# Kernel tuning notes

Measured on AMD Instinct MI355X. Metric: run time of the kernel, lower is better.

The kernel has to match this reference:

```python
import jax, jax.numpy as jnp
import numpy as np

N_NODES = 100000
N_EDGES = 600000
DIM_IN = 128
DIM_OUT = 40
N_LAYERS = 3


def setup_inputs() -> dict:
    key = jax.random.key(0)
    ks = jax.random.split(key, 6)
    x = jax.random.normal(ks[0], (N_NODES, DIM_IN), dtype=jnp.float32)
    edge_index = jax.random.randint(ks[1], (2, N_EDGES), 0, N_NODES, dtype=jnp.int64)
    eps = jnp.zeros((N_LAYERS,), dtype=jnp.float32)
    Ws = jax.random.normal(ks[2], (N_LAYERS, DIM_IN, DIM_IN), dtype=jnp.float32) * 0.08
    bs = jnp.zeros((N_LAYERS, DIM_IN), dtype=jnp.float32)
    W_head = jax.random.normal(ks[3], (DIM_IN, DIM_OUT), dtype=jnp.float32) * 0.08
    b_head = jnp.zeros((DIM_OUT,), dtype=jnp.float32)
    return {"x": x, "edge_index": edge_index, "eps": eps, "Ws": Ws,
            "bs": bs, "W_head": W_head, "b_head": b_head}


def reference(x, edge_index, eps, Ws, bs, W_head, b_head):
    # GINConv (train_eps): x' = Linear((1+eps)*x + sum_{j->i} x_j)
    src, dst = edge_index[0], edge_index[1]
    n = x.shape[0]
    for l in range(N_LAYERS):
        agg = jax.ops.segment_sum(x[src], dst, num_segments=n)  # scatter-add over edges
        x = ((1.0 + eps[l]) * x + agg) @ Ws[l] + bs[l]
        # dropout is identity in eval mode
    return x @ W_head + b_head  # node-level head Linear(dim_in, dim_out)
```

## Files before the change

kernel.cpp:

```cpp
#include <hip/hip_runtime.h>

#define DIM 128
#define NOUT 40

typedef __attribute__((ext_vector_type(8))) short bf16x8_t;
typedef __attribute__((ext_vector_type(4))) float f32x4_t;
typedef __attribute__((ext_vector_type(4))) unsigned u32x4_t;

__device__ __forceinline__ ushort f2bf(float f) {
    unsigned u = __float_as_uint(f);
    u += 0x7fffu + ((u >> 16) & 1u);
    return (ushort)(u >> 16);
}


__global__ __launch_bounds__(256) void hist_kernel(
    const int* __restrict__ dst, int* __restrict__ deg, int n_edges)
{
    int e = blockIdx.x * 256 + threadIdx.x;
    if (e < n_edges) atomicAdd(&deg[dst[e]], 1);
}

__global__ __launch_bounds__(256) void reduce_kernel(
    const int* __restrict__ deg, int* __restrict__ bsum, int n)
{
    int t = threadIdx.x;
    int base = blockIdx.x * 1024 + t;
    int s = 0;
    #pragma unroll
    for (int i = 0; i < 4; ++i) { int idx = base + i * 256; s += (idx < n) ? deg[idx] : 0; }
    for (int o = 32; o; o >>= 1) s += __shfl_down(s, o, 64);
    __shared__ int l[4];
    if ((t & 63) == 0) l[t >> 6] = s;
    __syncthreads();
    if (t == 0) bsum[blockIdx.x] = l[0] + l[1] + l[2] + l[3];
}

__global__ __launch_bounds__(128) void scan_sums_kernel(
    int* __restrict__ bsum, int nb, int* __restrict__ off_n)
{
    __shared__ int l[128];
    int t = threadIdx.x;
    int c = (nb + 127) >> 7;
    int b = t * c, e = min(b + c, nb);
    int s = 0;
    for (int i = b; i < e; ++i) s += bsum[i];
    l[t] = s;
    __syncthreads();
    for (int d = 1; d < 128; d <<= 1) {
        int u = (t >= d) ? l[t - d] : 0;
        __syncthreads();
        l[t] += u;
        __syncthreads();
    }
    int pre = l[t] - s;
    for (int i = b; i < e; ++i) { int v = bsum[i]; bsum[i] = pre; pre += v; }
    if (t == 127) *off_n = l[127];
}

__global__ __launch_bounds__(256) void apply_kernel(
    const int* __restrict__ deg, const int* __restrict__ bsum,
    int* __restrict__ off, int n)
{
    int t = threadIdx.x;
    int i0 = blockIdx.x * 1024 + t * 4;
    int d0 = (i0     < n) ? deg[i0]     : 0;
    int d1 = (i0 + 1 < n) ? deg[i0 + 1] : 0;
    int d2 = (i0 + 2 < n) ? deg[i0 + 2] : 0;
    int d3 = (i0 + 3 < n) ? deg[i0 + 3] : 0;
    int s = d0 + d1 + d2 + d3;
    int inc = s;
    for (int o = 1; o < 64; o <<= 1) {
        int u = __shfl_up(inc, o, 64);
        if ((t & 63) >= o) inc += u;
    }
    __shared__ int wt[4];
    if ((t & 63) == 63) wt[t >> 6] = inc;
    __syncthreads();
    int wpre = 0;
    #pragma unroll
    for (int i = 0; i < 4; ++i) wpre += (i < (t >> 6)) ? wt[i] : 0;
    int excl = bsum[blockIdx.x] + wpre + inc - s;
    if (i0     < n) off[i0]     = excl;
    if (i0 + 1 < n) off[i0 + 1] = excl + d0;
    if (i0 + 2 < n) off[i0 + 2] = excl + d0 + d1;
    if (i0 + 3 < n) off[i0 + 3] = excl + d0 + d1 + d2;
}

__global__ __launch_bounds__(256) void fill_kernel(
    const int* __restrict__ src, const int* __restrict__ dst,
    const int* __restrict__ off, int* __restrict__ cursor,
    int* __restrict__ csr_src, int n_edges)
{
    int e = blockIdx.x * 256 + threadIdx.x;
    if (e >= n_edges) return;
    int d = dst[e];
    int pos = off[d] + atomicAdd(&cursor[d], 1);
    csr_src[pos] = src[e];
}


__global__ __launch_bounds__(256) void cast_x_kernel(
    const float* __restrict__ x, ushort* __restrict__ xb, int n4)
{
    int i = blockIdx.x * 256 + threadIdx.x;
    if (i >= n4) return;
    float4 v = reinterpret_cast<const float4*>(x)[i];
    reinterpret_cast<ushort4*>(xb)[i] =
        make_ushort4(f2bf(v.x), f2bf(v.y), f2bf(v.z), f2bf(v.w));
}

__global__ __launch_bounds__(256) void pack_w_kernel(
    const float* __restrict__ Ws, const float* __restrict__ Wh,
    ushort* __restrict__ pW, ushort* __restrict__ pWh)
{
    int tid = blockIdx.x * 256 + threadIdx.x;
    if (tid < 3 * 16384) {
        int l = tid / 16384, r = tid % 16384;
        int j = r & 7, lane = (r >> 3) & 63, cb = (r >> 9) & 7, ks = r >> 12;
        int k  = ks * 32 + (lane >> 4) * 8 + j;
        int nn = cb * 16 + (lane & 15);
        pW[tid] = f2bf(Ws[(size_t)l * DIM * DIM + (size_t)k * DIM + nn]);
    } else {
        int r = tid - 3 * 16384;
        if (r < 4 * 3 * 64 * 8) {
            int j = r & 7, lane = (r >> 3) & 63;
            int rem = r >> 9;
            int cb = rem % 3, ks = rem / 3;
            int k  = ks * 32 + (lane >> 4) * 8 + j;
            int nn = cb * 16 + (lane & 15);
            pWh[r] = (nn < NOUT) ? f2bf(Wh[(size_t)k * NOUT + nn]) : (ushort)0;
        }
    }
}

template<bool HEAD>
__global__ __launch_bounds__(256) void gin_fused_mfma(
    const ushort* __restrict__ xb,
    const int* __restrict__ csr, const int* __restrict__ off,
    const ushort* __restrict__ pW, const float* __restrict__ bias,
    const ushort* __restrict__ pWh, const float* __restrict__ bh,
    const float* __restrict__ eps, int layer,
    ushort* __restrict__ Y, float* __restrict__ out, int n_nodes)
{
    __shared__ ushort lds[4][16][136];

    const int t = threadIdx.x, wave = t >> 6, lane = t & 63;
    const int rloc = lane & 15;
    const int kseg = lane >> 4;
    const int row16 = blockIdx.x * 64 + wave * 16;
    const int node  = row16 + rloc;
    const int nclamp = min(node, n_nodes - 1);
    const float e1 = 1.0f + eps[layer];

    float a[4][8];
    {
        const ushort* xr = xb + (size_t)nclamp * DIM + kseg * 8;
        #pragma unroll
        for (int s = 0; s < 4; ++s) {
            u32x4_t v = *reinterpret_cast<const u32x4_t*>(xr + s * 32);
            #pragma unroll
            for (int q = 0; q < 4; ++q) {
                a[s][2*q]   = e1 * __uint_as_float(v[q] << 16);
                a[s][2*q+1] = e1 * __uint_as_float(v[q] & 0xffff0000u);
            }
        }
    }
    int k = off[nclamp], ke = off[nclamp + 1];
    for (; k + 1 < ke; k += 2) {
        const ushort* r0 = xb + (size_t)csr[k]     * DIM + kseg * 8;
        const ushort* r1 = xb + (size_t)csr[k + 1] * DIM + kseg * 8;
        u32x4_t u0[4], u1[4];
        #pragma unroll
        for (int s = 0; s < 4; ++s) u0[s] = *reinterpret_cast<const u32x4_t*>(r0 + s * 32);
        #pragma unroll
        for (int s = 0; s < 4; ++s) u1[s] = *reinterpret_cast<const u32x4_t*>(r1 + s * 32);
        #pragma unroll
        for (int s = 0; s < 4; ++s)
            #pragma unroll
            for (int q = 0; q < 4; ++q) {
                a[s][2*q]   += __uint_as_float(u0[s][q] << 16)
                             + __uint_as_float(u1[s][q] << 16);
                a[s][2*q+1] += __uint_as_float(u0[s][q] & 0xffff0000u)
                             + __uint_as_float(u1[s][q] & 0xffff0000u);
            }
    }
    if (k < ke) {
        const ushort* r0 = xb + (size_t)csr[k] * DIM + kseg * 8;
        #pragma unroll
        for (int s = 0; s < 4; ++s) {
            u32x4_t v = *reinterpret_cast<const u32x4_t*>(r0 + s * 32);
            #pragma unroll
            for (int q = 0; q < 4; ++q) {
                a[s][2*q]   += __uint_as_float(v[q] << 16);
                a[s][2*q+1] += __uint_as_float(v[q] & 0xffff0000u);
            }
        }
    }

    bf16x8_t af[4];
    #pragma unroll
    for (int s = 0; s < 4; ++s)
        #pragma unroll
        for (int j = 0; j < 8; ++j) af[s][j] = (short)f2bf(a[s][j]);

    const bf16x8_t* pw8 = reinterpret_cast<const bf16x8_t*>(pW);
    f32x4_t acc[8];
    #pragma unroll
    for (int cb = 0; cb < 8; ++cb) acc[cb] = (f32x4_t)(bias[cb * 16 + rloc]);
    #pragma unroll
    for (int cb = 0; cb < 8; ++cb) {
        const bf16x8_t* bp = pw8 + cb * 64 + lane;
        acc[cb] = __builtin_amdgcn_mfma_f32_16x16x32_bf16(af[0], bp[0],    acc[cb], 0, 0, 0);
        acc[cb] = __builtin_amdgcn_mfma_f32_16x16x32_bf16(af[1], bp[512],  acc[cb], 0, 0, 0);
        acc[cb] = __builtin_amdgcn_mfma_f32_16x16x32_bf16(af[2], bp[1024], acc[cb], 0, 0, 0);
        acc[cb] = __builtin_amdgcn_mfma_f32_16x16x32_bf16(af[3], bp[1536], acc[cb], 0, 0, 0);
    }

    #pragma unroll
    for (int cb = 0; cb < 8; ++cb)
        #pragma unroll
        for (int r = 0; r < 4; ++r)
            lds[wave][kseg * 4 + r][cb * 16 + rloc] = f2bf(acc[cb][r]);
    __syncthreads();

    if (!HEAD) {
        #pragma unroll
        for (int p = 0; p < 4; ++p) {
            int rl = p * 4 + kseg;
            int row = row16 + rl;
            bf16x8_t v = *reinterpret_cast<const bf16x8_t*>(&lds[wave][rl][rloc * 8]);
            if (row < n_nodes)
                *reinterpret_cast<bf16x8_t*>(Y + (size_t)row * DIM + rloc * 8) = v;
        }
    } else {
        bf16x8_t hf[4];
        #pragma unroll
        for (int s = 0; s < 4; ++s)
            hf[s] = *reinterpret_cast<const bf16x8_t*>(&lds[wave][rloc][s * 32 + kseg * 8]);
        const bf16x8_t* ph8 = reinterpret_cast<const bf16x8_t*>(pWh);
        f32x4_t hacc[3];
        #pragma unroll
        for (int cb = 0; cb < 3; ++cb) {
            int col = cb * 16 + rloc;
            hacc[cb] = (f32x4_t)((col < NOUT) ? bh[col] : 0.f);
            const bf16x8_t* bp = ph8 + cb * 64 + lane;
            hacc[cb] = __builtin_amdgcn_mfma_f32_16x16x32_bf16(hf[0], bp[0],   hacc[cb], 0, 0, 0);
            hacc[cb] = __builtin_amdgcn_mfma_f32_16x16x32_bf16(hf[1], bp[192], hacc[cb], 0, 0, 0);
            hacc[cb] = __builtin_amdgcn_mfma_f32_16x16x32_bf16(hf[2], bp[384], hacc[cb], 0, 0, 0);
            hacc[cb] = __builtin_amdgcn_mfma_f32_16x16x32_bf16(hf[3], bp[576], hacc[cb], 0, 0, 0);
        }
        #pragma unroll
        for (int cb = 0; cb < 3; ++cb) {
            int col = cb * 16 + rloc;
            if (col < NOUT) {
                #pragma unroll
                for (int r = 0; r < 4; ++r) {
                    int row = row16 + kseg * 4 + r;
                    if (row < n_nodes) out[(size_t)row * NOUT + col] = hacc[cb][r];
                }
            }
        }
    }
}

extern "C" void kernel_launch(void* const* d_in, const int* in_sizes, int n_in,
                              void* d_out, int out_size, void* d_ws, size_t ws_size,
                              hipStream_t stream) {
    (void)n_in; (void)out_size; (void)ws_size;
    const float* x    = (const float*)d_in[0];
    const int*   edge = (const int*)d_in[1];
    const float* eps  = (const float*)d_in[2];
    const float* Ws   = (const float*)d_in[3];
    const float* bs   = (const float*)d_in[4];
    const float* Wh   = (const float*)d_in[5];
    const float* bh   = (const float*)d_in[6];

    const int n_nodes = in_sizes[0] / DIM;
    const int n_edges = in_sizes[1] / 2;
    const int* src = edge;
    const int* dst = edge + n_edges;

    const size_t halfE = (size_t)n_nodes * DIM;
    ushort* buf0 = (ushort*)d_ws;
    ushort* buf1 = buf0 + halfE;
    char* p = (char*)(buf1 + halfE);
    int* deg  = (int*)p;            p += (size_t)n_nodes * 4;
    int* off  = (int*)p;            p += ((size_t)n_nodes + 1) * 4;
    int* bsum = (int*)p;            p += 512;
    int* csr  = (int*)p;            p += (size_t)n_edges * 4;
    p = (char*)(((uintptr_t)p + 15) & ~(uintptr_t)15);
    ushort* pW  = (ushort*)p;       p += 3 * 16384 * 2;
    ushort* pWh = (ushort*)p;

    const dim3 blk(256);
    const int edge_grid  = (n_edges + 255) / 256;
    const int fused_grid = (n_nodes + 63) / 64;
    const int nscan = (n_nodes + 1023) / 1024;
    const int cast_n4 = n_nodes * DIM / 4;

    hipMemsetAsync(deg, 0, (size_t)n_nodes * sizeof(int), stream);
    hist_kernel<<<edge_grid, blk, 0, stream>>>(dst, deg, n_edges);
    reduce_kernel<<<nscan, blk, 0, stream>>>(deg, bsum, n_nodes);
    scan_sums_kernel<<<1, 128, 0, stream>>>(bsum, nscan, off + n_nodes);
    apply_kernel<<<nscan, blk, 0, stream>>>(deg, bsum, off, n_nodes);
    hipMemsetAsync(deg, 0, (size_t)n_nodes * sizeof(int), stream);
    fill_kernel<<<edge_grid, blk, 0, stream>>>(src, dst, off, deg, csr, n_edges);

    cast_x_kernel<<<(cast_n4 + 255) / 256, blk, 0, stream>>>(x, buf0, cast_n4);
    pack_w_kernel<<<(3 * 16384 + 4 * 3 * 64 * 8 + 255) / 256, blk, 0, stream>>>(Ws, Wh, pW, pWh);

    gin_fused_mfma<false><<<fused_grid, blk, 0, stream>>>(
        buf0, csr, off, pW,          bs,           pWh, bh, eps, 0, buf1, nullptr, n_nodes);
    gin_fused_mfma<false><<<fused_grid, blk, 0, stream>>>(
        buf1, csr, off, pW + 16384,  bs + DIM,     pWh, bh, eps, 1, buf0, nullptr, n_nodes);
    gin_fused_mfma<true><<<fused_grid, blk, 0, stream>>>(
        buf0, csr, off, pW + 32768,  bs + 2 * DIM, pWh, bh, eps, 2, nullptr, (float*)d_out, n_nodes);
}
```

Measured before the change: 222.8 us.

## Stage block edge lists in LDS, unroll gather by four, merge prep launches

Each fused GIN block now cooperatively loads its contiguous CSR edge-index range into shared memory and gathers neighbour rows four at a time instead of two, with a global-memory fallback when the range exceeds the LDS capacity. The cast and weight-pack kernels are merged into one launch, and the second deg memset is folded into apply_kernel, which zeroes deg after reading it. The aim is less dependent index-load latency and more memory-level parallelism in the gather, plus fewer launches. The extra LDS and the added sync may reduce occupancy.

```diff
diff --git a/kernel.cpp b/kernel.cpp
--- a/kernel.cpp
+++ b/kernel.cpp
@@ -2,6 +2,7 @@
 
 #define DIM 128
 #define NOUT 40
+#define ECAP 1152
 
 typedef __attribute__((ext_vector_type(8))) short bf16x8_t;
 typedef __attribute__((ext_vector_type(4))) float f32x4_t;
@@ -59,7 +60,7 @@
 }
 
 __global__ __launch_bounds__(256) void apply_kernel(
-    const int* __restrict__ deg, const int* __restrict__ bsum,
+    int* __restrict__ deg, const int* __restrict__ bsum,
     int* __restrict__ off, int n)
 {
     int t = threadIdx.x;
@@ -81,10 +82,10 @@
     #pragma unroll
     for (int i = 0; i < 4; ++i) wpre += (i < (t >> 6)) ? wt[i] : 0;
     int excl = bsum[blockIdx.x] + wpre + inc - s;
-    if (i0     < n) off[i0]     = excl;
-    if (i0 + 1 < n) off[i0 + 1] = excl + d0;
-    if (i0 + 2 < n) off[i0 + 2] = excl + d0 + d1;
-    if (i0 + 3 < n) off[i0 + 3] = excl + d0 + d1 + d2;
+    if (i0     < n) { off[i0]     = excl;                deg[i0]     = 0; }
+    if (i0 + 1 < n) { off[i0 + 1] = excl + d0;           deg[i0 + 1] = 0; }
+    if (i0 + 2 < n) { off[i0 + 2] = excl + d0 + d1;      deg[i0 + 2] = 0; }
+    if (i0 + 3 < n) { off[i0 + 3] = excl + d0 + d1 + d2; deg[i0 + 3] = 0; }
 }
 
 __global__ __launch_bounds__(256) void fill_kernel(
@@ -99,22 +100,19 @@
     csr_src[pos] = src[e];
 }
 
-
-__global__ __launch_bounds__(256) void cast_x_kernel(
-    const float* __restrict__ x, ushort* __restrict__ xb, int n4)
-{
-    int i = blockIdx.x * 256 + threadIdx.x;
-    if (i >= n4) return;
-    float4 v = reinterpret_cast<const float4*>(x)[i];
-    reinterpret_cast<ushort4*>(xb)[i] =
-        make_ushort4(f2bf(v.x), f2bf(v.y), f2bf(v.z), f2bf(v.w));
-}
-
-__global__ __launch_bounds__(256) void pack_w_kernel(
+__global__ __launch_bounds__(256) void prep_kernel(
+    const float* __restrict__ x, ushort* __restrict__ xb, int n4,
     const float* __restrict__ Ws, const float* __restrict__ Wh,
     ushort* __restrict__ pW, ushort* __restrict__ pWh)
 {
-    int tid = blockIdx.x * 256 + threadIdx.x;
+    int i = blockIdx.x * 256 + threadIdx.x;
+    if (i < n4) {
+        float4 v = reinterpret_cast<const float4*>(x)[i];
+        reinterpret_cast<ushort4*>(xb)[i] =
+            make_ushort4(f2bf(v.x), f2bf(v.y), f2bf(v.z), f2bf(v.w));
+        return;
+    }
+    int tid = i - n4;
     if (tid < 3 * 16384) {
         int l = tid / 16384, r = tid % 16384;
         int j = r & 7, lane = (r >> 3) & 63, cb = (r >> 9) & 7, ks = r >> 12;
@@ -134,6 +132,55 @@
     }
 }
 
+template<typename IP>
+__device__ __forceinline__ void gather_rows(
+    const ushort* __restrict__ xb, const IP idx,
+    int kb, int ke, int kofs, float a[4][8])
+{
+    int k = kb;
+    for (; k + 3 < ke; k += 4) {
+        int s0 = idx[k], s1 = idx[k + 1], s2 = idx[k + 2], s3 = idx[k + 3];
+        const ushort* r0 = xb + (size_t)s0 * DIM + kofs;
+        const ushort* r1 = xb + (size_t)s1 * DIM + kofs;
+        const ushort* r2 = xb + (size_t)s2 * DIM + kofs;
+        const ushort* r3 = xb + (size_t)s3 * DIM + kofs;
+        u32x4_t u0[4], u1[4], u2[4], u3[4];
+        #pragma unroll
+        for (int s = 0; s < 4; ++s) u0[s] = *reinterpret_cast<const u32x4_t*>(r0 + s * 32);
+        #pragma unroll
+        for (int s = 0; s < 4; ++s) u1[s] = *reinterpret_cast<const u32x4_t*>(r1 + s * 32);
+        #pragma unroll
+        for (int s = 0; s < 4; ++s) u2[s] = *reinterpret_cast<const u32x4_t*>(r2 + s * 32);
+        #pragma unroll
+        for (int s = 0; s < 4; ++s) u3[s] = *reinterpret_cast<const u32x4_t*>(r3 + s * 32);
+        #pragma unroll
+        for (int s = 0; s < 4; ++s)
+            #pragma unroll
+            for (int q = 0; q < 4; ++q) {
+                a[s][2*q]   += (__uint_as_float(u0[s][q] << 16)
+                              + __uint_as_float(u1[s][q] << 16))
+                             + (__uint_as_float(u2[s][q] << 16)
+                              + __uint_as_float(u3[s][q] << 16));
+                a[s][2*q+1] += (__uint_as_float(u0[s][q] & 0xffff0000u)
+                              + __uint_as_float(u1[s][q] & 0xffff0000u))
+                             + (__uint_as_float(u2[s][q] & 0xffff0000u)
+                              + __uint_as_float(u3[s][q] & 0xffff0000u));
+            }
+    }
+    for (; k < ke; ++k) {
+        const ushort* r0 = xb + (size_t)idx[k] * DIM + kofs;
+        #pragma unroll
+        for (int s = 0; s < 4; ++s) {
+            u32x4_t v = *reinterpret_cast<const u32x4_t*>(r0 + s * 32);
+            #pragma unroll
+            for (int q = 0; q < 4; ++q) {
+                a[s][2*q]   += __uint_as_float(v[q] << 16);
+                a[s][2*q+1] += __uint_as_float(v[q] & 0xffff0000u);
+            }
+        }
+    }
+}
+
 template<bool HEAD>
 __global__ __launch_bounds__(256) void gin_fused_mfma(
     const ushort* __restrict__ xb,
@@ -144,18 +191,29 @@
     ushort* __restrict__ Y, float* __restrict__ out, int n_nodes)
 {
     __shared__ ushort lds[4][16][136];
+    __shared__ int elist[ECAP];
 
     const int t = threadIdx.x, wave = t >> 6, lane = t & 63;
     const int rloc = lane & 15;
     const int kseg = lane >> 4;
-    const int row16 = blockIdx.x * 64 + wave * 16;
+    const int kofs = kseg * 8;
+    const int blkbase = (int)blockIdx.x * 64;
+    const int row16 = blkbase + wave * 16;
     const int node  = row16 + rloc;
     const int nclamp = min(node, n_nodes - 1);
     const float e1 = 1.0f + eps[layer];
 
+    const int blk_lo = off[min(blkbase, n_nodes)];
+    const int blk_hi = off[min(blkbase + 64, n_nodes)];
+    const int etot = blk_hi - blk_lo;
+    const bool use_lds = (etot <= ECAP);
+    if (use_lds)
+        for (int i = t; i < etot; i += 256) elist[i] = csr[blk_lo + i];
+    __syncthreads();
+
     float a[4][8];
     {
-        const ushort* xr = xb + (size_t)nclamp * DIM + kseg * 8;
+        const ushort* xr = xb + (size_t)nclamp * DIM + kofs;
         #pragma unroll
         for (int s = 0; s < 4; ++s) {
             u32x4_t v = *reinterpret_cast<const u32x4_t*>(xr + s * 32);
@@ -166,36 +224,10 @@
             }
         }
     }
-    int k = off[nclamp], ke = off[nclamp + 1];
-    for (; k + 1 < ke; k += 2) {
-        const ushort* r0 = xb + (size_t)csr[k]     * DIM + kseg * 8;
-        const ushort* r1 = xb + (size_t)csr[k + 1] * DIM + kseg * 8;
-        u32x4_t u0[4], u1[4];
-        #pragma unroll
-        for (int s = 0; s < 4; ++s) u0[s] = *reinterpret_cast<const u32x4_t*>(r0 + s * 32);
-        #pragma unroll
-        for (int s = 0; s < 4; ++s) u1[s] = *reinterpret_cast<const u32x4_t*>(r1 + s * 32);
-        #pragma unroll
-        for (int s = 0; s < 4; ++s)
-            #pragma unroll
-            for (int q = 0; q < 4; ++q) {
-                a[s][2*q]   += __uint_as_float(u0[s][q] << 16)
-                             + __uint_as_float(u1[s][q] << 16);
-                a[s][2*q+1] += __uint_as_float(u0[s][q] & 0xffff0000u)
-                             + __uint_as_float(u1[s][q] & 0xffff0000u);
-            }
-    }
-    if (k < ke) {
-        const ushort* r0 = xb + (size_t)csr[k] * DIM + kseg * 8;
-        #pragma unroll
-        for (int s = 0; s < 4; ++s) {
-            u32x4_t v = *reinterpret_cast<const u32x4_t*>(r0 + s * 32);
-            #pragma unroll
-            for (int q = 0; q < 4; ++q) {
-                a[s][2*q]   += __uint_as_float(v[q] << 16);
-                a[s][2*q+1] += __uint_as_float(v[q] & 0xffff0000u);
-            }
-        }
+    {
+        int kb = off[nclamp] - blk_lo, ke2 = off[nclamp + 1] - blk_lo;
+        if (use_lds) gather_rows(xb, (const int*)elist, kb, ke2, kofs, a);
+        else         gather_rows(xb, csr + blk_lo,      kb, ke2, kofs, a);
     }
 
     bf16x8_t af[4];
@@ -237,7 +269,7 @@
         bf16x8_t hf[4];
         #pragma unroll
         for (int s = 0; s < 4; ++s)
-            hf[s] = *reinterpret_cast<const bf16x8_t*>(&lds[wave][rloc][s * 32 + kseg * 8]);
+            hf[s] = *reinterpret_cast<const bf16x8_t*>(&lds[wave][rloc][s * 32 + kofs]);
         const bf16x8_t* ph8 = reinterpret_cast<const bf16x8_t*>(pWh);
         f32x4_t hacc[3];
         #pragma unroll
@@ -298,17 +330,17 @@
     const int fused_grid = (n_nodes + 63) / 64;
     const int nscan = (n_nodes + 1023) / 1024;
     const int cast_n4 = n_nodes * DIM / 4;
-
-    hipMemsetAsync(deg, 0, (size_t)n_nodes * sizeof(int), stream);
+    const int prep_items = cast_n4 + 3 * 16384 + 4 * 3 * 64 * 8;
+
+    (void)hipMemsetAsync(deg, 0, (size_t)n_nodes * sizeof(int), stream);
     hist_kernel<<<edge_grid, blk, 0, stream>>>(dst, deg, n_edges);
     reduce_kernel<<<nscan, blk, 0, stream>>>(deg, bsum, n_nodes);
     scan_sums_kernel<<<1, 128, 0, stream>>>(bsum, nscan, off + n_nodes);
     apply_kernel<<<nscan, blk, 0, stream>>>(deg, bsum, off, n_nodes);
-    hipMemsetAsync(deg, 0, (size_t)n_nodes * sizeof(int), stream);
     fill_kernel<<<edge_grid, blk, 0, stream>>>(src, dst, off, deg, csr, n_edges);
 
-    cast_x_kernel<<<(cast_n4 + 255) / 256, blk, 0, stream>>>(x, buf0, cast_n4);
-    pack_w_kernel<<<(3 * 16384 + 4 * 3 * 64 * 8 + 255) / 256, blk, 0, stream>>>(Ws, Wh, pW, pWh);
+    prep_kernel<<<(prep_items + 255) / 256, blk, 0, stream>>>(
+        x, buf0, cast_n4, Ws, Wh, pW, pWh);
 
     gin_fused_mfma<false><<<fused_grid, blk, 0, stream>>>(
         buf0, csr, off, pW,          bs,           pWh, bh, eps, 0, buf1, nullptr, n_nodes);
```

Result: no change. 225.8 us (+1.4%).
